# Optimization experiments

Hardware: AMD Instinct MI355X
Metric: run time of the kernel (lower is better)

## Reference

```python
import jax, jax.numpy as jnp
import numpy as np
from jax import lax

PATCH = 32  # enc conv kernel/stride
EPS = 1e-12  # F.normalize eps


def setup_inputs() -> dict:
    key = jax.random.key(0)
    ks = jax.random.split(key, 7)
    B, N, H, W = 32, 256, 32, 32
    fdim, vdim = 512, 128
    x = jax.random.normal(ks[0], (B, 3 * N, H, W), dtype=jnp.float32)
    conv_w = jax.random.normal(ks[1], (fdim, 3, PATCH, PATCH), dtype=jnp.float32) * (1.0 / np.sqrt(3 * PATCH * PATCH))
    conv_b = jax.random.normal(ks[2], (fdim,), dtype=jnp.float32) * 0.01
    fc1_w = jax.random.normal(ks[3], (vdim, fdim), dtype=jnp.float32) * (1.0 / np.sqrt(fdim))
    fc1_b = jax.random.normal(ks[4], (vdim,), dtype=jnp.float32) * 0.01
    # deterministic dropout masks (p=0.5, train mode -> keep * 1/(1-p))
    drop1 = (jax.random.uniform(ks[5], (B, N, N)) >= 0.5).astype(jnp.float32) * 2.0
    drop2 = (jax.random.uniform(ks[6], (B, N, N)) >= 0.5).astype(jnp.float32) * 2.0
    return {"x": x, "conv_w": conv_w, "conv_b": conv_b,
            "fc1_w": fc1_w, "fc1_b": fc1_b, "drop1": drop1, "drop2": drop2}


def _branch(scores, drop, eye):
    # softmax over dim=-2, zero diag, dropout, L1-normalize over dim=-2
    P = jax.nn.softmax(scores, axis=-2)
    P = P * (1.0 - eye)
    P = P * drop
    denom = jnp.maximum(jnp.sum(jnp.abs(P), axis=-2, keepdims=True), EPS)
    return P / denom


def reference(x, conv_w, conv_b, fc1_w, fc1_b, drop1, drop2):
    B, C, H, W = x.shape
    N = C // 3
    xi = x.reshape(B * N, 3, H, W)
    # enc: patchify conv -> (B*N, fdim, 1, 1)
    fm = lax.conv_general_dilated(xi, conv_w, (PATCH, PATCH), 'VALID',
                                  dimension_numbers=('NCHW', 'OIHW', 'NCHW'))
    fm = fm + conv_b[None, :, None, None]
    # map2vec: adaptive avgpool(1,1) + flatten + fc1
    v = fm.mean(axis=(2, 3))                      # (B*N, fdim)
    v = v @ fc1_w.T + fc1_b                       # (B*N, vdim)
    f = v.reshape(B, N, -1)                       # (B, N, vdim)
    f_norm = f / jnp.maximum(jnp.linalg.norm(f, axis=-1, keepdims=True), EPS)
    A = jnp.einsum('bnd,bmd->bnm', f_norm, f_norm)  # cosine affinity (B,N,N)
    Atemp = A * (128.0 ** 0.5)                    # torch.div(A, 1/128**0.5)
    eye = jnp.eye(N, dtype=A.dtype)
    A1 = _branch(Atemp, drop1, eye)
    A2t = _branch(jnp.swapaxes(Atemp, -1, -2), drop2, eye)
    AtA = jnp.swapaxes(jnp.matmul(A2t, A1), -1, -2)
    # nll_loss(AtA, arange targets) == -mean of diagonal entries
    diag = jnp.einsum('bii->bi', AtA)
    loss = -jnp.mean(diag)
    return f, A, loss
```

## Files before the change

### kernel.cpp

```cpp
#include <hip/hip_runtime.h>
#include <stdint.h>

#define S_SCALE 11.313708498984761f
#define EPS 1e-12f

typedef __bf16 bf16x8 __attribute__((ext_vector_type(8)));
typedef float  f32x4  __attribute__((ext_vector_type(4)));

__device__ __forceinline__ f32x4 mfma16(bf16x8 a, bf16x8 b, f32x4 c) {
  return __builtin_amdgcn_mfma_f32_16x16x32_bf16(a, b, c, 0, 0, 0);
}

__device__ __forceinline__ float waveSum(float v) {
#pragma unroll
  for (int m = 32; m > 0; m >>= 1) v += __shfl_xor(v, m, 64);
  return v;
}

__device__ __forceinline__ void load_lds16(const float* g, float* l) {
  __builtin_amdgcn_global_load_lds(
      (const __attribute__((address_space(1))) uint32_t*)g,
      (__attribute__((address_space(3))) uint32_t*)l, 16, 0, 0);
}

#define OFF_W    0
#define OFF_BIAS 786432
#define OFF_FN   786944
#define OFF_ZP   2884096
#define OFF_P1   3146240

__global__ __launch_bounds__(256) void k_bias(const float* __restrict__ fc1_w,
                                              const float* __restrict__ conv_b,
                                              const float* __restrict__ fc1_b,
                                              float* __restrict__ bias2,
                                              float* __restrict__ loss) {
  const int o = blockIdx.x, t = threadIdx.x;
  if (o == 0 && t == 0) loss[0] = 0.f;
  float p = fc1_w[o * 512 + t] * conv_b[t] +
            fc1_w[o * 512 + 256 + t] * conv_b[256 + t];
  p = waveSum(p);
  __shared__ float red[4];
  if ((t & 63) == 0) red[t >> 6] = p;
  __syncthreads();
  if (t == 0) bias2[o] = red[0] + red[1] + red[2] + red[3] + fc1_b[o];
}

__global__ __launch_bounds__(256) void k_fusew2(const float* __restrict__ conv_w,
                                                const float* __restrict__ fc1_w,
                                                __bf16* __restrict__ W) {
  __shared__ float cw_s[64][36];
  __shared__ float fc1_s[128][65];
  const int t = threadIdx.x;
  const int kt = blockIdx.x;
  const int k0 = kt * 32;
  const int og = t >> 3, kg = t & 7;
  float acc[4][4] = {};
  for (int cs = 0; cs < 8; ++cs) {
    const int cc = cs * 64;
    __syncthreads();
#pragma unroll
    for (int i = 0; i < 8; ++i) {
      int idx = t + 256 * i;
      int cr = idx >> 5, kk = idx & 31;
      cw_s[cr][kk] = conv_w[(cc + cr) * 3072 + k0 + kk];
    }
#pragma unroll
    for (int i = 0; i < 8; ++i) {
      int idx = t + 256 * i;
      int o = idx >> 4, c4 = (idx & 15) * 4;
      float4 v = *(const float4*)&fc1_w[o * 512 + cc + c4];
      fc1_s[o][c4 + 0] = v.x; fc1_s[o][c4 + 1] = v.y;
      fc1_s[o][c4 + 2] = v.z; fc1_s[o][c4 + 3] = v.w;
    }
    __syncthreads();
    for (int ci = 0; ci < 64; ++ci) {
      float4 cw = *(const float4*)&cw_s[ci][kg * 4];
#pragma unroll
      for (int j = 0; j < 4; ++j) {
        float fv = fc1_s[og * 4 + j][ci];
        acc[j][0] = fmaf(fv, cw.x, acc[j][0]);
        acc[j][1] = fmaf(fv, cw.y, acc[j][1]);
        acc[j][2] = fmaf(fv, cw.z, acc[j][2]);
        acc[j][3] = fmaf(fv, cw.w, acc[j][3]);
      }
    }
  }
#pragma unroll
  for (int j = 0; j < 4; ++j)
#pragma unroll
    for (int q = 0; q < 4; ++q)
      W[(og * 4 + j) * 3072 + k0 + kg * 4 + q] = (__bf16)acc[j][q];
}

__global__ __launch_bounds__(256) void k_gemm1(const float* __restrict__ x,
                                               const __bf16* __restrict__ W,
                                               float* __restrict__ P0,
                                               float* __restrict__ P1) {
  __shared__ __align__(16) float A_lds[32 * 64];
  const int t = threadIdx.x;
  const int wave = t >> 6, lane = t & 63;
  const int l15 = lane & 15, quad = lane >> 4;
  const int m0 = blockIdx.x * 32;
  const int kbase = blockIdx.y * 1536;
  float* P = blockIdx.y ? P1 : P0;

  int dr[2], dc[2];
#pragma unroll
  for (int j = 0; j < 2; ++j) {
    int row = wave * 8 + j * 4 + (lane >> 4);
    int cl = (lane & 15) ^ (row & 15);
    dr[j] = row;
    dc[j] = cl * 4;
  }

  f32x4 acc[2][2] = {{{0.f,0.f,0.f,0.f},{0.f,0.f,0.f,0.f}},
                     {{0.f,0.f,0.f,0.f},{0.f,0.f,0.f,0.f}}};
  const __bf16* bp = W + (wave * 32 + l15) * 3072 + quad * 8;

  for (int it = 0; it < 24; ++it) {
    const int k0 = kbase + it * 64;
    __syncthreads();
#pragma unroll
    for (int j = 0; j < 2; ++j)
      load_lds16(x + (m0 + dr[j]) * 3072 + k0 + dc[j],
                 &A_lds[(wave * 2 + j) * 256]);
    uint4 breg[2][2];
#pragma unroll
    for (int ks = 0; ks < 2; ++ks)
#pragma unroll
      for (int ni = 0; ni < 2; ++ni)
        breg[ks][ni] = *(const uint4*)(bp + ni * 16 * 3072 + k0 + ks * 32);
    __syncthreads();
#pragma unroll
    for (int ks = 0; ks < 2; ++ks) {
      bf16x8 afrag[2];
#pragma unroll
      for (int mi = 0; mi < 2; ++mi) {
        const int rb = (l15 + mi * 16) * 64;
        float4 lo = *(const float4*)&A_lds[rb + (((ks * 8 + quad * 2 + 0) ^ l15) << 2)];
        float4 hi = *(const float4*)&A_lds[rb + (((ks * 8 + quad * 2 + 1) ^ l15) << 2)];
        union { __bf16 h[8]; bf16x8 v; } pk;
        pk.h[0] = (__bf16)lo.x; pk.h[1] = (__bf16)lo.y;
        pk.h[2] = (__bf16)lo.z; pk.h[3] = (__bf16)lo.w;
        pk.h[4] = (__bf16)hi.x; pk.h[5] = (__bf16)hi.y;
        pk.h[6] = (__bf16)hi.z; pk.h[7] = (__bf16)hi.w;
        afrag[mi] = pk.v;
      }
#pragma unroll
      for (int mi = 0; mi < 2; ++mi)
#pragma unroll
        for (int ni = 0; ni < 2; ++ni)
          acc[mi][ni] = mfma16(afrag[mi], *(const bf16x8*)&breg[ks][ni],
                               acc[mi][ni]);
    }
  }
#pragma unroll
  for (int mi = 0; mi < 2; ++mi)
#pragma unroll
    for (int ni = 0; ni < 2; ++ni) {
      int col = wave * 32 + ni * 16 + l15;
#pragma unroll
      for (int r = 0; r < 4; ++r) {
        int row = m0 + mi * 16 + quad * 4 + r;
        P[row * 128 + col] = acc[mi][ni][r];
      }
    }
}

__global__ __launch_bounds__(256) void k_fin(float* __restrict__ f_inout,
                                             const float* __restrict__ P1,
                                             const float* __restrict__ bias2,
                                             __bf16* __restrict__ fn) {
  const int wave = threadIdx.x >> 6, lane = threadIdx.x & 63;
  const int row = blockIdx.x * 4 + wave;
  const int i0 = row * 128 + lane, i1 = i0 + 64;
  float v0 = f_inout[i0] + P1[i0] + bias2[lane];
  float v1 = f_inout[i1] + P1[i1] + bias2[lane + 64];
  float ss = waveSum(fmaf(v0, v0, v1 * v1));
  float inv = 1.f / fmaxf(sqrtf(ss), EPS);
  f_inout[i0] = v0;
  f_inout[i1] = v1;
  fn[i0] = (__bf16)(v0 * inv);
  fn[i1] = (__bf16)(v1 * inv);
}

__global__ __launch_bounds__(256) void k_gemm2(const __bf16* __restrict__ fn,
                                               const float* __restrict__ d1,
                                               const float* __restrict__ d2,
                                               float* __restrict__ Aout,
                                               float* __restrict__ Zp) {
  __shared__ __align__(16) __bf16 Li[64][136];
  __shared__ __align__(16) __bf16 Lj[64][136];
  __shared__ float zred[2][4][64];
  const int t = threadIdx.x;
  const int b = blockIdx.y;
  const int ti = blockIdx.x >> 2, tj = blockIdx.x & 3;
  const int i0 = ti * 64, j0 = tj * 64;
  const int wave = t >> 6, lane = t & 63;
  const int l15 = lane & 15, quad = lane >> 4;
  const __bf16* fb = fn + b * 32768;
#pragma unroll
  for (int i = 0; i < 4; ++i) {
    int idx = t + 256 * i;
    int r = idx >> 4, c8 = (idx & 15) * 8;
    *(uint4*)&Li[r][c8] = *(const uint4*)&fb[(i0 + r) * 128 + c8];
    *(uint4*)&Lj[r][c8] = *(const uint4*)&fb[(j0 + r) * 128 + c8];
  }
  __syncthreads();
  f32x4 acc[4] = {{0.f, 0.f, 0.f, 0.f}, {0.f, 0.f, 0.f, 0.f},
                  {0.f, 0.f, 0.f, 0.f}, {0.f, 0.f, 0.f, 0.f}};
#pragma unroll
  for (int ks = 0; ks < 4; ++ks) {
    bf16x8 af = *(const bf16x8*)&Li[wave * 16 + l15][ks * 32 + quad * 8];
#pragma unroll
    for (int nt = 0; nt < 4; ++nt) {
      bf16x8 bf = *(const bf16x8*)&Lj[nt * 16 + l15][ks * 32 + quad * 8];
      acc[nt] = mfma16(af, bf, acc[nt]);
    }
  }
  const int base = b * 65536;
  float* Ab = Aout + base;
  float z1c[4] = {0.f, 0.f, 0.f, 0.f}, z2c[4] = {0.f, 0.f, 0.f, 0.f};
#pragma unroll
  for (int nt = 0; nt < 4; ++nt) {
    int gj = j0 + nt * 16 + l15;
#pragma unroll
    for (int r = 0; r < 4; ++r) {
      int gi = i0 + wave * 16 + quad * 4 + r;
      float a = acc[nt][r];
      Ab[gi * 256 + gj] = a;
      float e = __expf(fmaf(S_SCALE, a, -S_SCALE));
      if (gi != gj) {
        int idx = base + gi * 256 + gj;
        z1c[nt] = fmaf(e, d1[idx], z1c[nt]);
        z2c[nt] = fmaf(e, d2[idx], z2c[nt]);
      }
    }
  }
#pragma unroll
  for (int nt = 0; nt < 4; ++nt) {
    z1c[nt] += __shfl_xor(z1c[nt], 16, 64);
    z1c[nt] += __shfl_xor(z1c[nt], 32, 64);
    z2c[nt] += __shfl_xor(z2c[nt], 16, 64);
    z2c[nt] += __shfl_xor(z2c[nt], 32, 64);
  }
  if (quad == 0) {
#pragma unroll
    for (int nt = 0; nt < 4; ++nt) {
      zred[0][wave][nt * 16 + l15] = z1c[nt];
      zred[1][wave][nt * 16 + l15] = z2c[nt];
    }
  }
  __syncthreads();
  if (t < 128) {
    int z = t >> 6, c = t & 63;
    float s = zred[z][0][c] + zred[z][1][c] + zred[z][2][c] + zred[z][3][c];
    Zp[(z * 4 + ti) * 8192 + b * 256 + j0 + c] = s;
  }
}

__global__ __launch_bounds__(256) void k_loss(const float* __restrict__ Aout,
                                              const float* __restrict__ d1,
                                              const float* __restrict__ d2,
                                              const float* __restrict__ Zp,
                                              float* __restrict__ loss) {
  __shared__ float d1s[64][65];
  __shared__ float z1s[64], z2s[64];
  __shared__ float red[4];
  const int t = threadIdx.x;
  const int b = blockIdx.y;
  const int ic = blockIdx.x >> 2, kc = blockIdx.x & 3;
  const int i0 = ic * 64, k0 = kc * 64;
  const int base = b * 65536;
  if (t < 64) {
    float s = 0.f;
#pragma unroll
    for (int p = 0; p < 4; ++p) s += Zp[p * 8192 + b * 256 + i0 + t];
    z1s[t] = 1.f / fmaxf(s, EPS);
  } else if (t < 128) {
    float s = 0.f;
#pragma unroll
    for (int p = 0; p < 4; ++p) s += Zp[(4 + p) * 8192 + b * 256 + k0 + t - 64];
    z2s[t - 64] = 1.f / fmaxf(s, EPS);
  }
#pragma unroll
  for (int ii = 0; ii < 16; ++ii) {
    int idx = t + 256 * ii;
    int kr = idx >> 6, ci = idx & 63;
    d1s[kr][ci] = d1[base + (k0 + kr) * 256 + i0 + ci];
  }
  __syncthreads();
  const int kl = t & 63, ig = t >> 6;
  float inv2 = z2s[kl];
  float accv = 0.f;
  for (int ii = 0; ii < 16; ++ii) {
    int il = ig * 16 + ii;
    int idx = base + (i0 + il) * 256 + k0 + kl;
    float a = Aout[idx];
    float e = __expf(fmaf(2.f * S_SCALE, a, -2.f * S_SCALE));
    float v = e * d2[idx] * d1s[kl][il] * z1s[il] * inv2;
    if (i0 + il != k0 + kl) accv += v;
  }
  accv = waveSum(accv);
  if ((t & 63) == 0) red[t >> 6] = accv;
  __syncthreads();
  if (t == 0) {
    float tot = red[0] + red[1] + red[2] + red[3];
    atomicAdd(loss, tot * (-1.f / 8192.f));
  }
}

extern "C" void kernel_launch(void* const* d_in, const int* in_sizes, int n_in,
                              void* d_out, int out_size, void* d_ws,
                              size_t ws_size, hipStream_t stream) {
  const float* x = (const float*)d_in[0];
  const float* conv_w = (const float*)d_in[1];
  const float* conv_b = (const float*)d_in[2];
  const float* fc1_w = (const float*)d_in[3];
  const float* fc1_b = (const float*)d_in[4];
  const float* drop1 = (const float*)d_in[5];
  const float* drop2 = (const float*)d_in[6];
  char* ws = (char*)d_ws;
  __bf16* W = (__bf16*)(ws + OFF_W);
  float* bias2 = (float*)(ws + OFF_BIAS);
  __bf16* fn = (__bf16*)(ws + OFF_FN);
  float* Zp = (float*)(ws + OFF_ZP);
  float* P1 = (float*)(ws + OFF_P1);
  float* f = (float*)d_out;
  float* Aout = f + 1048576;
  float* loss = f + 3145728;

  k_bias<<<128, 256, 0, stream>>>(fc1_w, conv_b, fc1_b, bias2, loss);
  k_fusew2<<<96, 256, 0, stream>>>(conv_w, fc1_w, W);
  k_gemm1<<<dim3(256, 2), 256, 0, stream>>>(x, W, f, P1);
  k_fin<<<2048, 256, 0, stream>>>(f, P1, bias2, fn);
  k_gemm2<<<dim3(16, 32), 256, 0, stream>>>(fn, drop1, drop2, Aout, Zp);
  k_loss<<<dim3(16, 32), 256, 0, stream>>>(Aout, drop1, drop2, Zp, loss);
}
```

Baseline: 238.8 us.

## Double-buffer gemm1 A tiles and merge bias and weight-fusion prep kernels

The first GEMM now keeps two LDS buffers for the x tile and two register sets for the W fragments. The loads for the next K step are issued before computing the current one, so global loads overlap with MFMA work, and each step needs one barrier instead of two. Separately, the bias kernel and the weight-fusion kernel are merged into a single launch that dispatches on block index, which removes one kernel launch. The cost is double the LDS and more registers in gemm1, which could lower occupancy.

```diff
diff --git a/kernel.cpp b/kernel.cpp
--- a/kernel.cpp
+++ b/kernel.cpp
@@ -29,28 +29,28 @@
 #define OFF_ZP   2884096
 #define OFF_P1   3146240
 
-__global__ __launch_bounds__(256) void k_bias(const float* __restrict__ fc1_w,
+__global__ __launch_bounds__(256) void k_prep(const float* __restrict__ conv_w,
+                                              const float* __restrict__ fc1_w,
                                               const float* __restrict__ conv_b,
                                               const float* __restrict__ fc1_b,
+                                              __bf16* __restrict__ W,
                                               float* __restrict__ bias2,
                                               float* __restrict__ loss) {
-  const int o = blockIdx.x, t = threadIdx.x;
-  if (o == 0 && t == 0) loss[0] = 0.f;
-  float p = fc1_w[o * 512 + t] * conv_b[t] +
-            fc1_w[o * 512 + 256 + t] * conv_b[256 + t];
-  p = waveSum(p);
-  __shared__ float red[4];
-  if ((t & 63) == 0) red[t >> 6] = p;
-  __syncthreads();
-  if (t == 0) bias2[o] = red[0] + red[1] + red[2] + red[3] + fc1_b[o];
-}
-
-__global__ __launch_bounds__(256) void k_fusew2(const float* __restrict__ conv_w,
-                                                const float* __restrict__ fc1_w,
-                                                __bf16* __restrict__ W) {
   __shared__ float cw_s[64][36];
   __shared__ float fc1_s[128][65];
+  __shared__ float red[4];
   const int t = threadIdx.x;
+  if (blockIdx.x >= 96) {
+    const int o = blockIdx.x - 96;
+    if (o == 0 && t == 0) loss[0] = 0.f;
+    float p = fc1_w[o * 512 + t] * conv_b[t] +
+              fc1_w[o * 512 + 256 + t] * conv_b[256 + t];
+    p = waveSum(p);
+    if ((t & 63) == 0) red[t >> 6] = p;
+    __syncthreads();
+    if (t == 0) bias2[o] = red[0] + red[1] + red[2] + red[3] + fc1_b[o];
+    return;
+  }
   const int kt = blockIdx.x;
   const int k0 = kt * 32;
   const int og = t >> 3, kg = t & 7;
@@ -92,11 +92,58 @@
       W[(og * 4 + j) * 3072 + k0 + kg * 4 + q] = (__bf16)acc[j][q];
 }
 
+__device__ __forceinline__ void stageA(const float* __restrict__ x,
+                                       float* __restrict__ lds, int wave,
+                                       const int dr[2], const int dc[2],
+                                       int m0, int k0) {
+#pragma unroll
+  for (int j = 0; j < 2; ++j)
+    load_lds16(x + (m0 + dr[j]) * 3072 + k0 + dc[j],
+               lds + (wave * 2 + j) * 256);
+}
+
+__device__ __forceinline__ void loadB(const __bf16* __restrict__ bp, int k0,
+                                      uint4 (&dst)[2][2]) {
+#pragma unroll
+  for (int ks = 0; ks < 2; ++ks)
+#pragma unroll
+    for (int ni = 0; ni < 2; ++ni)
+      dst[ks][ni] = *(const uint4*)(bp + ni * 16 * 3072 + k0 + ks * 32);
+}
+
+__device__ __forceinline__ void computeTile(const float* __restrict__ Abuf,
+                                            const uint4 (&breg)[2][2],
+                                            int l15, int quad,
+                                            f32x4 (&acc)[2][2]) {
+#pragma unroll
+  for (int ks = 0; ks < 2; ++ks) {
+    bf16x8 afrag[2];
+#pragma unroll
+    for (int mi = 0; mi < 2; ++mi) {
+      const int rb = (l15 + mi * 16) * 64;
+      float4 lo = *(const float4*)&Abuf[rb + (((ks * 8 + quad * 2 + 0) ^ l15) << 2)];
+      float4 hi = *(const float4*)&Abuf[rb + (((ks * 8 + quad * 2 + 1) ^ l15) << 2)];
+      union { __bf16 h[8]; bf16x8 v; } pk;
+      pk.h[0] = (__bf16)lo.x; pk.h[1] = (__bf16)lo.y;
+      pk.h[2] = (__bf16)lo.z; pk.h[3] = (__bf16)lo.w;
+      pk.h[4] = (__bf16)hi.x; pk.h[5] = (__bf16)hi.y;
+      pk.h[6] = (__bf16)hi.z; pk.h[7] = (__bf16)hi.w;
+      afrag[mi] = pk.v;
+    }
+#pragma unroll
+    for (int mi = 0; mi < 2; ++mi)
+#pragma unroll
+      for (int ni = 0; ni < 2; ++ni)
+        acc[mi][ni] = mfma16(afrag[mi], *(const bf16x8*)&breg[ks][ni],
+                             acc[mi][ni]);
+  }
+}
+
 __global__ __launch_bounds__(256) void k_gemm1(const float* __restrict__ x,
                                                const __bf16* __restrict__ W,
                                                float* __restrict__ P0,
                                                float* __restrict__ P1) {
-  __shared__ __align__(16) float A_lds[32 * 64];
+  __shared__ __align__(16) float A_lds[2][32 * 64];
   const int t = threadIdx.x;
   const int wave = t >> 6, lane = t & 63;
   const int l15 = lane & 15, quad = lane >> 4;
@@ -117,43 +164,27 @@
                      {{0.f,0.f,0.f,0.f},{0.f,0.f,0.f,0.f}}};
   const __bf16* bp = W + (wave * 32 + l15) * 3072 + quad * 8;
 
-  for (int it = 0; it < 24; ++it) {
-    const int k0 = kbase + it * 64;
-    __syncthreads();
-#pragma unroll
-    for (int j = 0; j < 2; ++j)
-      load_lds16(x + (m0 + dr[j]) * 3072 + k0 + dc[j],
-                 &A_lds[(wave * 2 + j) * 256]);
-    uint4 breg[2][2];
-#pragma unroll
-    for (int ks = 0; ks < 2; ++ks)
-#pragma unroll
-      for (int ni = 0; ni < 2; ++ni)
-        breg[ks][ni] = *(const uint4*)(bp + ni * 16 * 3072 + k0 + ks * 32);
-    __syncthreads();
-#pragma unroll
-    for (int ks = 0; ks < 2; ++ks) {
-      bf16x8 afrag[2];
-#pragma unroll
-      for (int mi = 0; mi < 2; ++mi) {
-        const int rb = (l15 + mi * 16) * 64;
-        float4 lo = *(const float4*)&A_lds[rb + (((ks * 8 + quad * 2 + 0) ^ l15) << 2)];
-        float4 hi = *(const float4*)&A_lds[rb + (((ks * 8 + quad * 2 + 1) ^ l15) << 2)];
-        union { __bf16 h[8]; bf16x8 v; } pk;
-        pk.h[0] = (__bf16)lo.x; pk.h[1] = (__bf16)lo.y;
-        pk.h[2] = (__bf16)lo.z; pk.h[3] = (__bf16)lo.w;
-        pk.h[4] = (__bf16)hi.x; pk.h[5] = (__bf16)hi.y;
-        pk.h[6] = (__bf16)hi.z; pk.h[7] = (__bf16)hi.w;
-        afrag[mi] = pk.v;
-      }
-#pragma unroll
-      for (int mi = 0; mi < 2; ++mi)
-#pragma unroll
-        for (int ni = 0; ni < 2; ++ni)
-          acc[mi][ni] = mfma16(afrag[mi], *(const bf16x8*)&breg[ks][ni],
-                               acc[mi][ni]);
-    }
-  }
+  uint4 bA[2][2], bB[2][2];
+  stageA(x, &A_lds[0][0], wave, dr, dc, m0, kbase);
+  loadB(bp, kbase, bA);
+  __syncthreads();
+
+  for (int it2 = 0; it2 < 12; ++it2) {
+    const int itA = it2 * 2;
+    stageA(x, &A_lds[1][0], wave, dr, dc, m0, kbase + (itA + 1) * 64);
+    loadB(bp, kbase + (itA + 1) * 64, bB);
+    __builtin_amdgcn_sched_barrier(0);
+    computeTile(&A_lds[0][0], bA, l15, quad, acc);
+    __syncthreads();
+    if (it2 < 11) {
+      stageA(x, &A_lds[0][0], wave, dr, dc, m0, kbase + (itA + 2) * 64);
+      loadB(bp, kbase + (itA + 2) * 64, bA);
+    }
+    __builtin_amdgcn_sched_barrier(0);
+    computeTile(&A_lds[1][0], bB, l15, quad, acc);
+    __syncthreads();
+  }
+
 #pragma unroll
   for (int mi = 0; mi < 2; ++mi)
 #pragma unroll
@@ -330,8 +361,7 @@
   float* Aout = f + 1048576;
   float* loss = f + 3145728;
 
-  k_bias<<<128, 256, 0, stream>>>(fc1_w, conv_b, fc1_b, bias2, loss);
-  k_fusew2<<<96, 256, 0, stream>>>(conv_w, fc1_w, W);
+  k_prep<<<224, 256, 0, stream>>>(conv_w, fc1_w, conv_b, fc1_b, W, bias2, loss);
   k_gemm1<<<dim3(256, 2), 256, 0, stream>>>(x, W, f, P1);
   k_fin<<<2048, 256, 0, stream>>>(f, P1, bias2, fn);
   k_gemm2<<<dim3(16, 32), 256, 0, stream>>>(fn, drop1, drop2, Aout, Zp);
```

After: 237.2 us. About the same (-0.7%).

## Double-buffer gemm1 with LDS-staged B tiles, 4-way split-K, merge prep kernels

Applied to the files above, without the earlier changes.

Restructures the feature GEMM to use 64x128 block tiles, staging both the fp32 input tile and the bf16 fused weight tile into LDS with swizzled direct global-to-LDS loads. It double-buffers these loads so the next K tile is fetched while the current one is computed. K is now split four ways instead of two, which writes three partial buffers that the finalize kernel sums. The bias and weight-fusion kernels are merged into one launch to drop one kernel's launch cost. In exchange, the partial-sum traffic in the finalize step grows and the GEMM uses more LDS per block.

```diff
diff --git a/kernel.cpp b/kernel.cpp
--- a/kernel.cpp
+++ b/kernel.cpp
@@ -17,7 +17,7 @@
   return v;
 }
 
-__device__ __forceinline__ void load_lds16(const float* g, float* l) {
+__device__ __forceinline__ void load_lds16(const void* g, void* l) {
   __builtin_amdgcn_global_load_lds(
       (const __attribute__((address_space(1))) uint32_t*)g,
       (__attribute__((address_space(3))) uint32_t*)l, 16, 0, 0);
@@ -27,30 +27,30 @@
 #define OFF_BIAS 786432
 #define OFF_FN   786944
 #define OFF_ZP   2884096
-#define OFF_P1   3146240
-
-__global__ __launch_bounds__(256) void k_bias(const float* __restrict__ fc1_w,
+#define OFF_P    3146240
+
+__global__ __launch_bounds__(256) void k_prep(const float* __restrict__ conv_w,
+                                              const float* __restrict__ fc1_w,
                                               const float* __restrict__ conv_b,
                                               const float* __restrict__ fc1_b,
+                                              __bf16* __restrict__ W,
                                               float* __restrict__ bias2,
                                               float* __restrict__ loss) {
-  const int o = blockIdx.x, t = threadIdx.x;
-  if (o == 0 && t == 0) loss[0] = 0.f;
-  float p = fc1_w[o * 512 + t] * conv_b[t] +
-            fc1_w[o * 512 + 256 + t] * conv_b[256 + t];
-  p = waveSum(p);
-  __shared__ float red[4];
-  if ((t & 63) == 0) red[t >> 6] = p;
-  __syncthreads();
-  if (t == 0) bias2[o] = red[0] + red[1] + red[2] + red[3] + fc1_b[o];
-}
-
-__global__ __launch_bounds__(256) void k_fusew2(const float* __restrict__ conv_w,
-                                                const float* __restrict__ fc1_w,
-                                                __bf16* __restrict__ W) {
   __shared__ float cw_s[64][36];
   __shared__ float fc1_s[128][65];
+  __shared__ float red[4];
   const int t = threadIdx.x;
+  if (blockIdx.x >= 96) {
+    const int o = blockIdx.x - 96;
+    if (o == 0 && t == 0) loss[0] = 0.f;
+    float p = fc1_w[o * 512 + t] * conv_b[t] +
+              fc1_w[o * 512 + 256 + t] * conv_b[256 + t];
+    p = waveSum(p);
+    if ((t & 63) == 0) red[t >> 6] = p;
+    __syncthreads();
+    if (t == 0) bias2[o] = red[0] + red[1] + red[2] + red[3] + fc1_b[o];
+    return;
+  }
   const int kt = blockIdx.x;
   const int k0 = kt * 32;
   const int og = t >> 3, kg = t & 7;
@@ -92,53 +92,61 @@
       W[(og * 4 + j) * 3072 + k0 + kg * 4 + q] = (__bf16)acc[j][q];
 }
 
-__global__ __launch_bounds__(256) void k_gemm1(const float* __restrict__ x,
-                                               const __bf16* __restrict__ W,
-                                               float* __restrict__ P0,
-                                               float* __restrict__ P1) {
-  __shared__ __align__(16) float A_lds[32 * 64];
+__global__ __launch_bounds__(256, 2) void k_gemm1(const float* __restrict__ x,
+                                                  const __bf16* __restrict__ W,
+                                                  float* __restrict__ f,
+                                                  float* __restrict__ P123) {
+  __shared__ __align__(16) float A_lds[2][64 * 64];
+  __shared__ __align__(16) __bf16 B_lds[2][128 * 64];
   const int t = threadIdx.x;
   const int wave = t >> 6, lane = t & 63;
+  const int wm = wave >> 1, wn = wave & 1;
   const int l15 = lane & 15, quad = lane >> 4;
-  const int m0 = blockIdx.x * 32;
-  const int kbase = blockIdx.y * 1536;
-  float* P = blockIdx.y ? P1 : P0;
-
-  int dr[2], dc[2];
-#pragma unroll
-  for (int j = 0; j < 2; ++j) {
-    int row = wave * 8 + j * 4 + (lane >> 4);
-    int cl = (lane & 15) ^ (row & 15);
-    dr[j] = row;
-    dc[j] = cl * 4;
-  }
-
-  f32x4 acc[2][2] = {{{0.f,0.f,0.f,0.f},{0.f,0.f,0.f,0.f}},
-                     {{0.f,0.f,0.f,0.f},{0.f,0.f,0.f,0.f}}};
-  const __bf16* bp = W + (wave * 32 + l15) * 3072 + quad * 8;
-
-  for (int it = 0; it < 24; ++it) {
-    const int k0 = kbase + it * 64;
-    __syncthreads();
-#pragma unroll
-    for (int j = 0; j < 2; ++j)
-      load_lds16(x + (m0 + dr[j]) * 3072 + k0 + dc[j],
-                 &A_lds[(wave * 2 + j) * 256]);
-    uint4 breg[2][2];
-#pragma unroll
-    for (int ks = 0; ks < 2; ++ks)
-#pragma unroll
-      for (int ni = 0; ni < 2; ++ni)
-        breg[ks][ni] = *(const uint4*)(bp + ni * 16 * 3072 + k0 + ks * 32);
-    __syncthreads();
+  const int m0 = blockIdx.x * 64;
+  const int q = blockIdx.y;
+  const int kbase = q * 768;
+  float* P = q == 0 ? f : P123 + (q - 1) * 1048576;
+
+  int adr[4], adc[4];
+#pragma unroll
+  for (int j = 0; j < 4; ++j) {
+    int row = (wave * 4 + j) * 4 + (lane >> 4);
+    adr[j] = row;
+    adc[j] = ((lane & 15) ^ (row & 15)) * 4;
+  }
+  int bo[4], bk[4];
+#pragma unroll
+  for (int j = 0; j < 4; ++j) {
+    int o = (wave * 4 + j) * 8 + (lane >> 3);
+    bo[j] = o;
+    bk[j] = ((lane & 7) ^ (o & 7)) * 8;
+  }
+
+  f32x4 acc[2][4] = {};
+
+  auto stage = [&](int kt, int buf) {
+    const int k0 = kbase + kt * 64;
+#pragma unroll
+    for (int j = 0; j < 4; ++j)
+      load_lds16(x + (m0 + adr[j]) * 3072 + k0 + adc[j],
+                 &A_lds[buf][(wave * 4 + j) * 256]);
+#pragma unroll
+    for (int j = 0; j < 4; ++j)
+      load_lds16(W + bo[j] * 3072 + k0 + bk[j],
+                 &B_lds[buf][(wave * 4 + j) * 512]);
+  };
+
+  auto compute = [&](int buf) {
+    const float* Abuf = &A_lds[buf][0];
+    const __bf16* Bbuf = &B_lds[buf][0];
 #pragma unroll
     for (int ks = 0; ks < 2; ++ks) {
       bf16x8 afrag[2];
 #pragma unroll
       for (int mi = 0; mi < 2; ++mi) {
-        const int rb = (l15 + mi * 16) * 64;
-        float4 lo = *(const float4*)&A_lds[rb + (((ks * 8 + quad * 2 + 0) ^ l15) << 2)];
-        float4 hi = *(const float4*)&A_lds[rb + (((ks * 8 + quad * 2 + 1) ^ l15) << 2)];
+        const int rb = (wm * 32 + mi * 16 + l15) * 64;
+        float4 lo = *(const float4*)&Abuf[rb + (((ks * 8 + quad * 2 + 0) ^ l15) << 2)];
+        float4 hi = *(const float4*)&Abuf[rb + (((ks * 8 + quad * 2 + 1) ^ l15) << 2)];
         union { __bf16 h[8]; bf16x8 v; } pk;
         pk.h[0] = (__bf16)lo.x; pk.h[1] = (__bf16)lo.y;
         pk.h[2] = (__bf16)lo.z; pk.h[3] = (__bf16)lo.w;
@@ -147,35 +155,50 @@
         afrag[mi] = pk.v;
       }
 #pragma unroll
-      for (int mi = 0; mi < 2; ++mi)
-#pragma unroll
-        for (int ni = 0; ni < 2; ++ni)
-          acc[mi][ni] = mfma16(afrag[mi], *(const bf16x8*)&breg[ks][ni],
-                               acc[mi][ni]);
-    }
-  }
+      for (int ni = 0; ni < 4; ++ni) {
+        const int o = wn * 64 + ni * 16 + l15;
+        bf16x8 bfrag =
+            *(const bf16x8*)&Bbuf[o * 64 + (((ks * 4 + quad) ^ (o & 7)) << 3)];
+#pragma unroll
+        for (int mi = 0; mi < 2; ++mi)
+          acc[mi][ni] = mfma16(afrag[mi], bfrag, acc[mi][ni]);
+      }
+    }
+  };
+
+  stage(0, 0);
+  __syncthreads();
+  for (int kt = 0; kt < 12; ++kt) {
+    if (kt < 11) stage(kt + 1, (kt + 1) & 1);
+    __builtin_amdgcn_sched_barrier(0);
+    compute(kt & 1);
+    __syncthreads();
+  }
+
 #pragma unroll
   for (int mi = 0; mi < 2; ++mi)
 #pragma unroll
-    for (int ni = 0; ni < 2; ++ni) {
-      int col = wave * 32 + ni * 16 + l15;
+    for (int ni = 0; ni < 4; ++ni) {
+      const int col = wn * 64 + ni * 16 + l15;
 #pragma unroll
       for (int r = 0; r < 4; ++r) {
-        int row = m0 + mi * 16 + quad * 4 + r;
+        const int row = m0 + wm * 32 + mi * 16 + quad * 4 + r;
         P[row * 128 + col] = acc[mi][ni][r];
       }
     }
 }
 
 __global__ __launch_bounds__(256) void k_fin(float* __restrict__ f_inout,
-                                             const float* __restrict__ P1,
+                                             const float* __restrict__ P123,
                                              const float* __restrict__ bias2,
                                              __bf16* __restrict__ fn) {
   const int wave = threadIdx.x >> 6, lane = threadIdx.x & 63;
   const int row = blockIdx.x * 4 + wave;
   const int i0 = row * 128 + lane, i1 = i0 + 64;
-  float v0 = f_inout[i0] + P1[i0] + bias2[lane];
-  float v1 = f_inout[i1] + P1[i1] + bias2[lane + 64];
+  float v0 = f_inout[i0] + P123[i0] + P123[1048576 + i0] +
+             P123[2097152 + i0] + bias2[lane];
+  float v1 = f_inout[i1] + P123[i1] + P123[1048576 + i1] +
+             P123[2097152 + i1] + bias2[lane + 64];
   float ss = waveSum(fmaf(v0, v0, v1 * v1));
   float inv = 1.f / fmaxf(sqrtf(ss), EPS);
   f_inout[i0] = v0;
@@ -325,15 +348,14 @@
   float* bias2 = (float*)(ws + OFF_BIAS);
   __bf16* fn = (__bf16*)(ws + OFF_FN);
   float* Zp = (float*)(ws + OFF_ZP);
-  float* P1 = (float*)(ws + OFF_P1);
+  float* P123 = (float*)(ws + OFF_P);
   float* f = (float*)d_out;
   float* Aout = f + 1048576;
   float* loss = f + 3145728;
 
-  k_bias<<<128, 256, 0, stream>>>(fc1_w, conv_b, fc1_b, bias2, loss);
-  k_fusew2<<<96, 256, 0, stream>>>(conv_w, fc1_w, W);
-  k_gemm1<<<dim3(256, 2), 256, 0, stream>>>(x, W, f, P1);
-  k_fin<<<2048, 256, 0, stream>>>(f, P1, bias2, fn);
+  k_prep<<<224, 256, 0, stream>>>(conv_w, fc1_w, conv_b, fc1_b, W, bias2, loss);
+  k_gemm1<<<dim3(128, 4), 256, 0, stream>>>(x, W, f, P123);
+  k_fin<<<2048, 256, 0, stream>>>(f, P123, bias2, fn);
   k_gemm2<<<dim3(16, 32), 256, 0, stream>>>(fn, drop1, drop2, Aout, Zp);
   k_loss<<<dim3(16, 32), 256, 0, stream>>>(Aout, drop1, drop2, Zp, loss);
 }
```

Result: no change. 236.0 us (-1.2%).
